# Kernel tuning notes

Hardware: AMD Instinct MI355X
Metric: run time of the kernel (lower is better)

The kernel has to match this reference:

```python
import jax, jax.numpy as jnp
import numpy as np

B = 16384
F_IN = 768
F_OUT = 512

def setup_inputs() -> dict:
    key = jax.random.key(0)
    k1, k2, k3, k4, k5, k6 = jax.random.split(key, 6)
    # densified sparse multi-hot boards (post to_dense())
    stm = jax.random.uniform(k1, (B, F_IN), dtype=jnp.float32)
    nstm = jax.random.uniform(k2, (B, F_IN), dtype=jnp.float32)
    s1 = 1.0 / np.sqrt(F_IN)
    s2 = 1.0 / np.sqrt(2 * F_OUT)
    W1 = jax.random.normal(k3, (F_OUT, F_IN), dtype=jnp.float32) * s1
    b1 = jax.random.normal(k4, (F_OUT,), dtype=jnp.float32) * s1
    W2 = jax.random.normal(k5, (1, 2 * F_OUT), dtype=jnp.float32) * s2
    b2 = jax.random.normal(k6, (1,), dtype=jnp.float32) * s2
    return {"stm": stm, "nstm": nstm, "W1": W1, "b1": b1, "W2": W2, "b2": b2}

def reference(stm, nstm, W1, b1, W2, b2):
    # shared feature transformer applied to both perspectives
    stm_p = stm @ W1.T + b1    # [B, F_OUT]
    nstm_p = nstm @ W1.T + b1  # [B, F_OUT]
    hidden = jnp.clip(jnp.concatenate((stm_p, nstm_p), axis=1), 0.0, 1.0)  # [B, 2*F_OUT]
    return jax.nn.sigmoid(hidden @ W2.T + b2)  # [B, 1]
```

## Files before the change

kernel.cpp:

```cpp
#include <hip/hip_runtime.h>
#include <hip/hip_bf16.h>

#define BATCH 16384
#define FIN   768
#define FOUT  512

#define BM 128
#define BN 128
#define BK 64
#define LDKA 72
#define NT (FIN / BK)
#define W1B_OFF 65536

typedef __attribute__((ext_vector_type(8))) short short8;
typedef __attribute__((ext_vector_type(4))) float floatx4;

__device__ __forceinline__ unsigned int cvt_pk_bf16(float a, float b) {
    unsigned int r;
    asm("v_cvt_pk_bf16_f32 %0, %1, %2" : "=v"(r) : "v"(a), "v"(b));
    return r;
}

__device__ __forceinline__ uint2 pack4(float4 v) {
    uint2 o;
    o.x = cvt_pk_bf16(v.x, v.y);
    o.y = cvt_pk_bf16(v.z, v.w);
    return o;
}

__device__ __forceinline__ void load_lds_16(const void* g, void* l) {
    __builtin_amdgcn_global_load_lds(
        (const __attribute__((address_space(1))) unsigned int*)g,
        (__attribute__((address_space(3))) unsigned int*)l,
        16, 0, 0);
}

__global__ __launch_bounds__(256) void cvt_w1(
    const float* __restrict__ W1, unsigned short* __restrict__ W1b)
{
    int base = (blockIdx.x * 256 + threadIdx.x) * 8;
    float4 a = *(const float4*)(W1 + base);
    float4 b = *(const float4*)(W1 + base + 4);
    uint2 pa = pack4(a), pb = pack4(b);
    uint4 o; o.x = pa.x; o.y = pa.y; o.z = pb.x; o.w = pb.y;
    *(uint4*)(W1b + base) = o;
}

__global__ __launch_bounds__(256, 4) void pn_gemm(
    const float* __restrict__ stm, const float* __restrict__ nstm,
    const unsigned short* __restrict__ W1b, const float* __restrict__ b1,
    const float* __restrict__ W2, float* __restrict__ ws)
{
    __shared__ __align__(16) unsigned short As[BM * LDKA];
    __shared__ __align__(16) unsigned short Bs[BN * BK];

    const int tid  = threadIdx.x;
    const int lane = tid & 63;
    const int wave = tid >> 6;
    const int wm   = wave >> 1;
    const int wn   = wave & 1;
    const int quad = lane >> 4;
    const int l16  = lane & 15;

    const int id = blockIdx.x;
    const int g  = id >> 5;
    const int w5 = id & 31;
    const int rowTileIdx = g * 8 + (w5 & 7);
    const int colTile    = (w5 >> 3) * BN;
    const int rowTile    = rowTileIdx * BM;

    const int p = (rowTile >= BATCH) ? 1 : 0;
    const float* __restrict__ X = p ? nstm : stm;
    const int rowOff = rowTile - p * BATCH;

    const int arow = tid >> 4;
    const int asp4 = tid & 15;
    const float* aPtr = X + (size_t)(rowOff + arow) * FIN + asp4 * 4;

    const int bRowInJ = lane >> 3;
    const int bgc     = (lane & 7) ^ bRowInJ;

    floatx4 acc[4][4];
    #pragma unroll
    for (int i = 0; i < 4; ++i)
        #pragma unroll
        for (int j = 0; j < 4; ++j)
            acc[i][j] = (floatx4)0.0f;

    for (int t = 0; t < NT; ++t) {
        const int kt = t * BK;
        __syncthreads();

        #pragma unroll
        for (int i = 0; i < 4; ++i) {
            const int J = wave + i * 4;
            const int row = J * 8 + bRowInJ;
            load_lds_16(W1b + (size_t)(colTile + row) * FIN + kt + bgc * 8,
                        &Bs[J * 512]);
        }
        #pragma unroll
        for (int i = 0; i < 8; ++i) {
            float4 v = *(const float4*)(aPtr + kt + (size_t)(i * 16) * FIN);
            *(uint2*)(&As[(arow + i * 16) * LDKA + asp4 * 4]) = pack4(v);
        }
        __syncthreads();

        #pragma unroll
        for (int s = 0; s < 2; ++s) {
            short8 af[4], bfr[4];
            #pragma unroll
            for (int mi = 0; mi < 4; ++mi)
                af[mi] = *(const short8*)(
                    &As[(wm * 64 + mi * 16 + l16) * LDKA + s * 32 + quad * 8]);
            #pragma unroll
            for (int ni = 0; ni < 4; ++ni) {
                const int r = wn * 64 + ni * 16 + l16;
                bfr[ni] = *(const short8*)(
                    &Bs[r * 64 + (((s * 4 + quad) ^ (r & 7)) * 8)]);
            }
            #pragma unroll
            for (int mi = 0; mi < 4; ++mi)
                #pragma unroll
                for (int ni = 0; ni < 4; ++ni)
                    acc[mi][ni] = __builtin_amdgcn_mfma_f32_16x16x32_bf16(
                        af[mi], bfr[ni], acc[mi][ni], 0, 0, 0);
        }
    }

    float b1v[4], w2v[4];
    #pragma unroll
    for (int ni = 0; ni < 4; ++ni) {
        int col = colTile + wn * 64 + ni * 16 + l16;
        b1v[ni] = b1[col];
        w2v[ni] = W2[p * FOUT + col];
    }

    const int rBase = rowOff + wm * 64;
    #pragma unroll
    for (int mi = 0; mi < 4; ++mi) {
        #pragma unroll
        for (int r = 0; r < 4; ++r) {
            float s = 0.0f;
            #pragma unroll
            for (int ni = 0; ni < 4; ++ni) {
                float h = acc[mi][ni][r] + b1v[ni];
                h = fminf(fmaxf(h, 0.0f), 1.0f);
                s += h * w2v[ni];
            }
            s += __shfl_xor(s, 1);
            s += __shfl_xor(s, 2);
            s += __shfl_xor(s, 4);
            s += __shfl_xor(s, 8);
            if (l16 == 0) {
                atomicAdd(&ws[rBase + mi * 16 + quad * 4 + r], s);
            }
        }
    }
}

__global__ __launch_bounds__(256) void pn_finalize(
    const float* __restrict__ ws, const float* __restrict__ b2,
    float* __restrict__ out)
{
    int i = blockIdx.x * blockDim.x + threadIdx.x;
    float x = ws[i] + b2[0];
    out[i] = 1.0f / (1.0f + expf(-x));
}

extern "C" void kernel_launch(void* const* d_in, const int* in_sizes, int n_in,
                              void* d_out, int out_size, void* d_ws, size_t ws_size,
                              hipStream_t stream)
{
    (void)in_sizes; (void)n_in; (void)out_size; (void)ws_size;
    const float* stm  = (const float*)d_in[0];
    const float* nstm = (const float*)d_in[1];
    const float* W1   = (const float*)d_in[2];
    const float* b1   = (const float*)d_in[3];
    const float* W2   = (const float*)d_in[4];
    const float* b2   = (const float*)d_in[5];
    float* out = (float*)d_out;
    float* ws  = (float*)d_ws;
    unsigned short* W1b = (unsigned short*)((char*)d_ws + W1B_OFF);

    hipMemsetAsync(ws, 0, BATCH * sizeof(float), stream);
    cvt_w1<<<dim3((FOUT * FIN) / (256 * 8)), dim3(256), 0, stream>>>(W1, W1b);

    dim3 grid((FOUT / BN) * ((2 * BATCH) / BM));
    pn_gemm<<<grid, dim3(256), 0, stream>>>(stm, nstm, W1b, b1, W2, ws);
    pn_finalize<<<dim3(BATCH / 256), dim3(256), 0, stream>>>(ws, b2, out);
}
```

Baseline: 161.6 us.

## Use 1024-thread blocks covering all outputs per batch slice and fuse the epilogue

Each block now handles 64 batch rows from both stm and nstm (128 A rows) across all 512 output columns with 16 waves. The W2 reduction and sigmoid finish in-block through LDS, which removes the atomics, the memset and the separate finalize kernel. A is register-prefetched one k-tile ahead and stored with an XOR swizzle. Each A element is now read once instead of once per column tile. The cost is 1024-thread blocks with 80KB LDS, so occupancy is lower, and each block reloads the whole W1 from L2.

```diff
diff --git a/kernel.cpp b/kernel.cpp
--- a/kernel.cpp
+++ b/kernel.cpp
@@ -5,12 +5,8 @@
 #define FIN   768
 #define FOUT  512
 
-#define BM 128
-#define BN 128
 #define BK 64
-#define LDKA 72
 #define NT (FIN / BK)
-#define W1B_OFF 65536
 
 typedef __attribute__((ext_vector_type(8))) short short8;
 typedef __attribute__((ext_vector_type(4))) float floatx4;
@@ -19,13 +15,6 @@
     unsigned int r;
     asm("v_cvt_pk_bf16_f32 %0, %1, %2" : "=v"(r) : "v"(a), "v"(b));
     return r;
-}
-
-__device__ __forceinline__ uint2 pack4(float4 v) {
-    uint2 o;
-    o.x = cvt_pk_bf16(v.x, v.y);
-    o.y = cvt_pk_bf16(v.z, v.w);
-    return o;
 }
 
 __device__ __forceinline__ void load_lds_16(const void* g, void* l) {
@@ -41,44 +30,41 @@
     int base = (blockIdx.x * 256 + threadIdx.x) * 8;
     float4 a = *(const float4*)(W1 + base);
     float4 b = *(const float4*)(W1 + base + 4);
-    uint2 pa = pack4(a), pb = pack4(b);
-    uint4 o; o.x = pa.x; o.y = pa.y; o.z = pb.x; o.w = pb.y;
+    uint4 o;
+    o.x = cvt_pk_bf16(a.x, a.y); o.y = cvt_pk_bf16(a.z, a.w);
+    o.z = cvt_pk_bf16(b.x, b.y); o.w = cvt_pk_bf16(b.z, b.w);
     *(uint4*)(W1b + base) = o;
 }
 
-__global__ __launch_bounds__(256, 4) void pn_gemm(
+__global__ __launch_bounds__(1024, 4) void pn_gemm(
     const float* __restrict__ stm, const float* __restrict__ nstm,
     const unsigned short* __restrict__ W1b, const float* __restrict__ b1,
-    const float* __restrict__ W2, float* __restrict__ ws)
+    const float* __restrict__ W2, const float* __restrict__ b2,
+    float* __restrict__ out)
 {
-    __shared__ __align__(16) unsigned short As[BM * LDKA];
-    __shared__ __align__(16) unsigned short Bs[BN * BK];
+    __shared__ __align__(16) unsigned short As[128 * 64];
+    __shared__ __align__(16) unsigned short Bs[512 * 64];
 
     const int tid  = threadIdx.x;
     const int lane = tid & 63;
     const int wave = tid >> 6;
-    const int wm   = wave >> 1;
-    const int wn   = wave & 1;
+    const int wrow = wave >> 3;
+    const int wcol = wave & 7;
     const int quad = lane >> 4;
     const int l16  = lane & 15;
+    const int l7   = l16 & 7;
 
-    const int id = blockIdx.x;
-    const int g  = id >> 5;
-    const int w5 = id & 31;
-    const int rowTileIdx = g * 8 + (w5 & 7);
-    const int colTile    = (w5 >> 3) * BN;
-    const int rowTile    = rowTileIdx * BM;
+    const int b0 = blockIdx.x * 64;
 
-    const int p = (rowTile >= BATCH) ? 1 : 0;
-    const float* __restrict__ X = p ? nstm : stm;
-    const int rowOff = rowTile - p * BATCH;
+    const int arow = wave * 8 + (lane & 7);
+    const int ac   = lane >> 3;
+    const float* aSrc = (arow < 64)
+        ? stm  + (size_t)(b0 + arow)      * FIN + ac * 8
+        : nstm + (size_t)(b0 + arow - 64) * FIN + ac * 8;
+    unsigned short* aDst = &As[arow * 64 + (ac ^ (arow & 7)) * 8];
 
-    const int arow = tid >> 4;
-    const int asp4 = tid & 15;
-    const float* aPtr = X + (size_t)(rowOff + arow) * FIN + asp4 * 4;
-
-    const int bRowInJ = lane >> 3;
-    const int bgc     = (lane & 7) ^ bRowInJ;
+    const int brl  = lane >> 3;
+    const int bg   = (lane & 7) ^ brl;
 
     floatx4 acc[4][4];
     #pragma unroll
@@ -87,21 +73,28 @@
         for (int j = 0; j < 4; ++j)
             acc[i][j] = (floatx4)0.0f;
 
+    float4 ap0 = *(const float4*)(aSrc);
+    float4 ap1 = *(const float4*)(aSrc + 4);
+
     for (int t = 0; t < NT; ++t) {
         const int kt = t * BK;
         __syncthreads();
 
         #pragma unroll
         for (int i = 0; i < 4; ++i) {
-            const int J = wave + i * 4;
-            const int row = J * 8 + bRowInJ;
-            load_lds_16(W1b + (size_t)(colTile + row) * FIN + kt + bgc * 8,
-                        &Bs[J * 512]);
+            const int row = i * 128 + wave * 8 + brl;
+            load_lds_16(W1b + (size_t)row * FIN + kt + bg * 8,
+                        &Bs[(i * 128 + wave * 8) * 64]);
         }
-        #pragma unroll
-        for (int i = 0; i < 8; ++i) {
-            float4 v = *(const float4*)(aPtr + kt + (size_t)(i * 16) * FIN);
-            *(uint2*)(&As[(arow + i * 16) * LDKA + asp4 * 4]) = pack4(v);
+        {
+            uint4 o;
+            o.x = cvt_pk_bf16(ap0.x, ap0.y); o.y = cvt_pk_bf16(ap0.z, ap0.w);
+            o.z = cvt_pk_bf16(ap1.x, ap1.y); o.w = cvt_pk_bf16(ap1.z, ap1.w);
+            *(uint4*)aDst = o;
+        }
+        if (t + 1 < NT) {
+            ap0 = *(const float4*)(aSrc + kt + BK);
+            ap1 = *(const float4*)(aSrc + kt + BK + 4);
         }
         __syncthreads();
 
@@ -109,14 +102,14 @@
         for (int s = 0; s < 2; ++s) {
             short8 af[4], bfr[4];
             #pragma unroll
-            for (int mi = 0; mi < 4; ++mi)
-                af[mi] = *(const short8*)(
-                    &As[(wm * 64 + mi * 16 + l16) * LDKA + s * 32 + quad * 8]);
+            for (int mi = 0; mi < 4; ++mi) {
+                const int m = wrow * 64 + mi * 16 + l16;
+                af[mi] = *(const short8*)(&As[m * 64 + ((s * 4 + quad) ^ l7) * 8]);
+            }
             #pragma unroll
             for (int ni = 0; ni < 4; ++ni) {
-                const int r = wn * 64 + ni * 16 + l16;
-                bfr[ni] = *(const short8*)(
-                    &Bs[r * 64 + (((s * 4 + quad) ^ (r & 7)) * 8)]);
+                const int n = wcol * 64 + ni * 16 + l16;
+                bfr[ni] = *(const short8*)(&Bs[n * 64 + ((s * 4 + quad) ^ l7) * 8]);
             }
             #pragma unroll
             for (int mi = 0; mi < 4; ++mi)
@@ -130,12 +123,14 @@
     float b1v[4], w2v[4];
     #pragma unroll
     for (int ni = 0; ni < 4; ++ni) {
-        int col = colTile + wn * 64 + ni * 16 + l16;
+        int col = wcol * 64 + ni * 16 + l16;
         b1v[ni] = b1[col];
-        w2v[ni] = W2[p * FOUT + col];
+        w2v[ni] = W2[wrow * FOUT + col];
     }
 
-    const int rBase = rowOff + wm * 64;
+    __syncthreads();
+    float* Epi = (float*)As;
+
     #pragma unroll
     for (int mi = 0; mi < 4; ++mi) {
         #pragma unroll
@@ -152,19 +147,19 @@
             s += __shfl_xor(s, 4);
             s += __shfl_xor(s, 8);
             if (l16 == 0) {
-                atomicAdd(&ws[rBase + mi * 16 + quad * 4 + r], s);
+                Epi[(wrow * 64 + mi * 16 + quad * 4 + r) * 8 + wcol] = s;
             }
         }
     }
-}
+    __syncthreads();
 
-__global__ __launch_bounds__(256) void pn_finalize(
-    const float* __restrict__ ws, const float* __restrict__ b2,
-    float* __restrict__ out)
-{
-    int i = blockIdx.x * blockDim.x + threadIdx.x;
-    float x = ws[i] + b2[0];
-    out[i] = 1.0f / (1.0f + expf(-x));
+    if (tid < 64) {
+        float x = b2[0];
+        #pragma unroll
+        for (int j = 0; j < 8; ++j)
+            x += Epi[tid * 8 + j] + Epi[(tid + 64) * 8 + j];
+        out[b0 + tid] = 1.0f / (1.0f + expf(-x));
+    }
 }
 
 extern "C" void kernel_launch(void* const* d_in, const int* in_sizes, int n_in,
@@ -179,13 +174,9 @@
     const float* W2   = (const float*)d_in[4];
     const float* b2   = (const float*)d_in[5];
     float* out = (float*)d_out;
-    float* ws  = (float*)d_ws;
-    unsigned short* W1b = (unsigned short*)((char*)d_ws + W1B_OFF);
+    unsigned short* W1b = (unsigned short*)d_ws;
 
-    hipMemsetAsync(ws, 0, BATCH * sizeof(float), stream);
     cvt_w1<<<dim3((FOUT * FIN) / (256 * 8)), dim3(256), 0, stream>>>(W1, W1b);
-
-    dim3 grid((FOUT / BN) * ((2 * BATCH) / BM));
-    pn_gemm<<<grid, dim3(256), 0, stream>>>(stm, nstm, W1b, b1, W2, ws);
-    pn_finalize<<<dim3(BATCH / 256), dim3(256), 0, stream>>>(ws, b2, out);
+    pn_gemm<<<dim3(BATCH / 64), dim3(1024), 0, stream>>>(
+        stm, nstm, W1b, b1, W2, b2, out);
 }
```

Result: faster. 153.5 us (-5.0%).
